# Kernel tuning notes

Measured on AMD Instinct MI355X. Metric: run time of the kernel, lower is better.

The kernel has to match this reference:

```python
import jax, jax.numpy as jnp
import numpy as np

ALPHA = 0.5
ITERATIONS = 10
N_CLASSES = 64


def setup_inputs() -> dict:
    key = jax.random.key(0)
    k1, k2, k3, k4 = jax.random.split(key, 4)
    d_in, d_emb = 512, 256
    n_support, n_query = 4096, 4096
    support = jax.random.normal(k1, (1, n_support, d_in), dtype=jnp.float32)
    query = jax.random.normal(k2, (1, n_query, d_in), dtype=jnp.float32)
    # encoder weight, scaled like a typical init so embeddings are O(1)
    W = jax.random.normal(k3, (d_in, d_emb), dtype=jnp.float32) / np.sqrt(d_in)
    support_labels = jax.random.randint(k4, (n_support,), 0, N_CLASSES, dtype=jnp.int64)
    return {"support": support, "query": query, "W": W, "support_labels": support_labels}


def reference(support, query, W, support_labels):
    n_support = support.shape[1]
    n_query = query.shape[1]
    d_in = support.shape[-1]

    # encoder: flatten episode dim, linear projection
    support_emb = support.reshape(-1, d_in) @ W        # [n_support, d_emb]
    query_emb = query.reshape(-1, d_in) @ W            # [n_query, d_emb]
    all_emb = jnp.concatenate([support_emb, query_emb], axis=0)  # [N, d_emb]

    # similarity graph and row-normalized adjacency
    similarity = all_emb @ all_emb.T                   # [N, N]
    adjacency = (similarity > 0.5).astype(jnp.float32)
    degree = adjacency.sum(axis=1, keepdims=True)
    degree = jnp.where(degree == 0, 1.0, degree)
    normalized = adjacency / degree                    # [N, N]

    # initial label matrix: one-hot for support rows, zeros for query rows
    support_onehot = jax.nn.one_hot(support_labels, N_CLASSES, dtype=jnp.float32)
    label_init = jnp.concatenate(
        [support_onehot, jnp.zeros((n_query, N_CLASSES), dtype=jnp.float32)], axis=0
    )  # [N, C]

    def step(_, labels):
        return (1.0 - ALPHA) * labels + ALPHA * (normalized @ labels)

    labels = jax.lax.fori_loop(0, ITERATIONS, step, label_init)
    query_labels = labels[n_support:]                  # [n_query, C]
    return query_labels
```

## Files before the change

kernel.cpp:

```cpp
#include <hip/hip_runtime.h>

#define NSUP 4096
#define NTOT 8192
#define DIN  512
#define DEMB 256
#define NCLS 64
#define PKS  8

typedef __attribute__((ext_vector_type(8))) short bf16x8;
typedef __attribute__((ext_vector_type(4))) float f32x4;
typedef __attribute__((ext_vector_type(4))) unsigned int u32x4;

__device__ inline unsigned short f2bf(float x) {
  unsigned int u = __builtin_bit_cast(unsigned int, x);
  u += 0x7FFFu + ((u >> 16) & 1u);
  return (unsigned short)(u >> 16);
}
__device__ inline float bf2f(unsigned short h) {
  unsigned int u = ((unsigned int)h) << 16;
  return __builtin_bit_cast(float, u);
}

__device__ inline size_t lfrag(int i, int c) {
  return (((size_t)(i >> 5) * (NCLS / 16) + (c >> 4)) * 64 +
          (c & 15) + 16 * ((i >> 3) & 3)) * 8 + (i & 7);
}

__global__ __launch_bounds__(256) void splitX(
    const float* __restrict__ support, const float* __restrict__ query,
    unsigned short* __restrict__ XhF, unsigned short* __restrict__ XlF) {
  int w = threadIdx.x >> 6, lane = threadIdx.x & 63;
  int row = blockIdx.x * 4 + w;
  const float* X = (row < NSUP) ? (support + (size_t)row * DIN)
                                : (query + (size_t)(row - NSUP) * DIN);
  const float4* p = (const float4*)(X + lane * 8);
  float4 a = p[0], b = p[1];
  float v[8] = {a.x, a.y, a.z, a.w, b.x, b.y, b.z, b.w};
  bf16x8 hv, lv;
  #pragma unroll
  for (int j = 0; j < 8; j++) {
    unsigned short h = f2bf(v[j]);
    hv[j] = (short)h;
    lv[j] = (short)f2bf(v[j] - bf2f(h));
  }
  size_t off = (((size_t)(row >> 4) * (DIN / 32) + (lane >> 2)) * 64 +
                (row & 15) + 16 * (lane & 3)) * 8;
  *reinterpret_cast<bf16x8*>(XhF + off) = hv;
  *reinterpret_cast<bf16x8*>(XlF + off) = lv;
}

__global__ __launch_bounds__(256) void splitW(
    const float* __restrict__ W, unsigned short* __restrict__ WhF,
    unsigned short* __restrict__ WlF) {
  int idx = blockIdx.x * 256 + threadIdx.x;
  int n = idx & 255, kb8 = idx >> 8;
  bf16x8 hv, lv;
  #pragma unroll
  for (int j = 0; j < 8; j++) {
    float v = W[(size_t)(kb8 * 8 + j) * DEMB + n];
    unsigned short h = f2bf(v);
    hv[j] = (short)h;
    lv[j] = (short)f2bf(v - bf2f(h));
  }
  size_t off = (((size_t)(n >> 4) * (DIN / 32) + (kb8 >> 2)) * 64 +
                (n & 15) + 16 * (kb8 & 3)) * 8;
  *reinterpret_cast<bf16x8*>(WhF + off) = hv;
  *reinterpret_cast<bf16x8*>(WlF + off) = lv;
}

__global__ __launch_bounds__(256) void emb_mfma(
    const unsigned short* __restrict__ XhF, const unsigned short* __restrict__ XlF,
    const unsigned short* __restrict__ WhF, const unsigned short* __restrict__ WlF,
    unsigned short* __restrict__ ehiF, unsigned short* __restrict__ eloF) {
  __shared__ float lds[4][16][65];
  int lane = threadIdx.x & 63, w = threadIdx.x >> 6;
  int l15 = lane & 15, lg = lane >> 4;
  int rowblk0 = blockIdx.x * 2;
  f32x4 acc[2][4] = {};
  for (int kb = 0; kb < DIN / 32; kb++) {
    bf16x8 ah[2], al[2], bh[4], bl[4];
    #pragma unroll
    for (int fm = 0; fm < 2; fm++) {
      size_t o = (((size_t)(rowblk0 + fm) * (DIN / 32) + kb) * 64 + lane) * 8;
      ah[fm] = *reinterpret_cast<const bf16x8*>(XhF + o);
      al[fm] = *reinterpret_cast<const bf16x8*>(XlF + o);
    }
    #pragma unroll
    for (int fn = 0; fn < 4; fn++) {
      size_t o = (((size_t)(w * 4 + fn) * (DIN / 32) + kb) * 64 + lane) * 8;
      bh[fn] = *reinterpret_cast<const bf16x8*>(WhF + o);
      bl[fn] = *reinterpret_cast<const bf16x8*>(WlF + o);
    }
    #pragma unroll
    for (int fm = 0; fm < 2; fm++)
      #pragma unroll
      for (int fn = 0; fn < 4; fn++) {
        acc[fm][fn] = __builtin_amdgcn_mfma_f32_16x16x32_bf16(ah[fm], bh[fn], acc[fm][fn], 0, 0, 0);
        acc[fm][fn] = __builtin_amdgcn_mfma_f32_16x16x32_bf16(ah[fm], bl[fn], acc[fm][fn], 0, 0, 0);
        acc[fm][fn] = __builtin_amdgcn_mfma_f32_16x16x32_bf16(al[fm], bh[fn], acc[fm][fn], 0, 0, 0);
        acc[fm][fn] = __builtin_amdgcn_mfma_f32_16x16x32_bf16(al[fm], bl[fn], acc[fm][fn], 0, 0, 0);
      }
  }
  for (int fm = 0; fm < 2; fm++) {
    #pragma unroll
    for (int fn = 0; fn < 4; fn++)
      #pragma unroll
      for (int r = 0; r < 4; r++)
        lds[w][lg * 4 + r][fn * 16 + l15] = acc[fm][fn][r];
    __syncthreads();
    #pragma unroll
    for (int cb = 0; cb < 2; cb++) {
      const float* src = &lds[w][l15][cb * 32 + lg * 8];
      bf16x8 hv, lv;
      #pragma unroll
      for (int j = 0; j < 8; j++) {
        float v = src[j];
        unsigned short h = f2bf(v);
        hv[j] = (short)h;
        lv[j] = (short)f2bf(v - bf2f(h));
      }
      size_t off = (((size_t)(rowblk0 + fm) * (DEMB / 32) + w * 2 + cb) * 64 + lane) * 8;
      *reinterpret_cast<bf16x8*>(ehiF + off) = hv;
      *reinterpret_cast<bf16x8*>(eloF + off) = lv;
    }
    __syncthreads();
  }
}

__global__ __launch_bounds__(256) void sim_kernel(
    const unsigned short* __restrict__ ehiF, const unsigned short* __restrict__ eloF,
    unsigned int* __restrict__ Apk) {
  int bid = (blockIdx.x & 7) * 260 + (blockIdx.x >> 3);
  int r = 2079 - bid;
  int j = (int)((sqrtf((float)(8 * r + 1)) - 1.0f) * 0.5f);
  while ((j + 1) * (j + 2) / 2 <= r) ++j;
  while (j * (j + 1) / 2 > r) --j;
  int by = 63 - j;
  int bx = 63 - (r - j * (j + 1) / 2);

  __shared__ unsigned short LTn[128][8];
  __shared__ unsigned short LTt[128][8];
  int lane = threadIdx.x & 63;
  int w = threadIdx.x >> 6, wm = w >> 1, wn = w & 1;
  int l15 = lane & 15, lg = lane >> 4;
  int arb = by * 8 + wm * 4, brb = bx * 8 + wn * 4;

  f32x4 acc[4][4] = {};
  #pragma unroll 2
  for (int kb = 0; kb < DEMB / 32; kb++) {
    bf16x8 bh[4], bl[4];
    #pragma unroll
    for (int fn = 0; fn < 4; fn++) {
      size_t o = (((size_t)(brb + fn) * (DEMB / 32) + kb) * 64 + lane) * 8;
      bh[fn] = *reinterpret_cast<const bf16x8*>(ehiF + o);
      bl[fn] = *reinterpret_cast<const bf16x8*>(eloF + o);
    }
    #pragma unroll
    for (int fm = 0; fm < 4; fm++) {
      size_t o = (((size_t)(arb + fm) * (DEMB / 32) + kb) * 64 + lane) * 8;
      bf16x8 ah = *reinterpret_cast<const bf16x8*>(ehiF + o);
      bf16x8 al = *reinterpret_cast<const bf16x8*>(eloF + o);
      #pragma unroll
      for (int fn = 0; fn < 4; fn++) {
        acc[fm][fn] = __builtin_amdgcn_mfma_f32_16x16x32_bf16(ah, bh[fn], acc[fm][fn], 0, 0, 0);
        acc[fm][fn] = __builtin_amdgcn_mfma_f32_16x16x32_bf16(ah, bl[fn], acc[fm][fn], 0, 0, 0);
        acc[fm][fn] = __builtin_amdgcn_mfma_f32_16x16x32_bf16(al, bh[fn], acc[fm][fn], 0, 0, 0);
      }
    }
  }
  #pragma unroll
  for (int fm = 0; fm < 4; fm++)
    #pragma unroll
    for (int fn = 0; fn < 4; fn++)
      #pragma unroll
      for (int r4 = 0; r4 < 4; r4++) {
        unsigned long long bal = __ballot(acc[fm][fn][r4] > 0.5f);
        if (l15 == 0)
          LTn[wm * 64 + fm * 16 + lg * 4 + r4][wn * 4 + fn] =
              (unsigned short)(bal >> (lg * 16));
      }
  __syncthreads();
  if (threadIdx.x < 64) {
    int tr = threadIdx.x >> 3, tc = threadIdx.x & 7;
    unsigned int m[16], t;
    #pragma unroll
    for (int q = 0; q < 16; q++) m[q] = LTn[tr * 16 + q][tc];
    #pragma unroll
    for (int i = 0; i < 8; i++) { t = ((m[i] >> 8) ^ m[i + 8]) & 0x00FFu; m[i + 8] ^= t; m[i] ^= t << 8; }
    #pragma unroll
    for (int g = 0; g < 16; g += 8)
      #pragma unroll
      for (int i = g; i < g + 4; i++) { t = ((m[i] >> 4) ^ m[i + 4]) & 0x0F0Fu; m[i + 4] ^= t; m[i] ^= t << 4; }
    #pragma unroll
    for (int g = 0; g < 16; g += 4)
      #pragma unroll
      for (int i = g; i < g + 2; i++) { t = ((m[i] >> 2) ^ m[i + 2]) & 0x3333u; m[i + 2] ^= t; m[i] ^= t << 2; }
    #pragma unroll
    for (int g = 0; g < 16; g += 2) { t = ((m[g] >> 1) ^ m[g + 1]) & 0x5555u; m[g + 1] ^= t; m[g] ^= t << 1; }
    #pragma unroll
    for (int q = 0; q < 16; q++) LTt[tc * 16 + q][tr] = (unsigned short)m[q];
  }
  __syncthreads();
  #pragma unroll
  for (int pass = 0; pass < 2; pass++) {
    int idx = pass * 256 + threadIdx.x;
    int rb4 = idx >> 6, ln = idx & 63;
    int lr = rb4 * 16 + (ln & 15), Lg = ln >> 4;
    unsigned int d = 0, d2 = 0;
    #pragma unroll
    for (int t = 0; t < 4; t++) {
      int bix = t * 4 + Lg;
      unsigned int u = LTn[lr][bix >> 1];
      d |= ((u >> ((bix & 1) * 8)) & 0xffu) << (t * 8);
      unsigned int u2 = LTt[lr][bix >> 1];
      d2 |= ((u2 >> ((bix & 1) * 8)) & 0xffu) << (t * 8);
    }
    Apk[((size_t)(by * 8 + rb4) * 64 + bx) * 64 + ln] = d;
    Apk[((size_t)(bx * 8 + rb4) * 64 + by) * 64 + ln] = d2;
  }
}

__global__ __launch_bounds__(256) void degree_kernel(
    const unsigned int* __restrict__ Apk, float* __restrict__ rdeg) {
  __shared__ int dg[4][16];
  int rowblk = blockIdx.x;
  int w = threadIdx.x >> 6, lane = threadIdx.x & 63;
  const unsigned int* base = Apk + (size_t)rowblk * 4096;
  int cnt = 0;
  #pragma unroll
  for (int s = 0; s < 16; s++) cnt += __popc(base[(w * 16 + s) * 64 + lane]);
  cnt += __shfl_xor(cnt, 16);
  cnt += __shfl_xor(cnt, 32);
  if (lane < 16) dg[w][lane] = cnt;
  __syncthreads();
  if (threadIdx.x < 16) {
    int c = dg[0][threadIdx.x] + dg[1][threadIdx.x] + dg[2][threadIdx.x] + dg[3][threadIdx.x];
    rdeg[rowblk * 16 + threadIdx.x] = (c == 0) ? 1.f : 1.f / (float)c;
  }
}

__global__ __launch_bounds__(256) void init_labels(
    const int* __restrict__ slab, float* __restrict__ labels,
    unsigned short* __restrict__ LtF) {
  int idx = blockIdx.x * 256 + threadIdx.x;
  int i = idx >> 6, c = idx & 63;
  float v = 0.f;
  if (i < NSUP && slab[i] == c) v = 1.f;
  labels[idx] = v;
  LtF[lfrag(i, c)] = f2bf(v);
}

#define RED(k, row, col) red[k][row][(col) ^ ((((row) >> 2) & 3) << 4)]
__global__ __launch_bounds__(512, 4) void prop_gemm(
    const unsigned int* __restrict__ Apk, const unsigned short* __restrict__ LtinF,
    float* __restrict__ Cpart) {
  __shared__ float red[4][64][64];
  int lane = threadIdx.x & 63;
  int w = threadIdx.x >> 6;
  int wr = w >> 2, wk = w & 3;
  int l15 = lane & 15, lg = lane >> 4;
  int ks = blockIdx.x, rg = blockIdx.y;
  int rb0 = rg * 8 + wr * 4;
  int s4base = ks * 8 + wk * 2;

  f32x4 acc[4][4] = {};
  #pragma unroll
  for (int s4 = 0; s4 < 2; s4++) {
    unsigned int ad[4];
    #pragma unroll
    for (int rb = 0; rb < 4; rb++)
      ad[rb] = Apk[((size_t)(rb0 + rb) * 64 + (s4base + s4)) * 64 + lane];
    #pragma unroll
    for (int t = 0; t < 4; t++) {
      int kstep = (s4base + s4) * 4 + t;
      bf16x8 b[4];
      #pragma unroll
      for (int fn = 0; fn < 4; fn++)
        b[fn] = *reinterpret_cast<const bf16x8*>(
            LtinF + (((size_t)kstep * 4 + fn) * 64 + lane) * 8);
      #pragma unroll
      for (int rb = 0; rb < 4; rb++) {
        unsigned int bb = (ad[rb] >> (8 * t)) & 0xffu;
        u32x4 uu;
        uu.x = ((bb & 1u)   ? 0x3F80u : 0u) | ((bb & 2u)   ? 0x3F800000u : 0u);
        uu.y = ((bb & 4u)   ? 0x3F80u : 0u) | ((bb & 8u)   ? 0x3F800000u : 0u);
        uu.z = ((bb & 16u)  ? 0x3F80u : 0u) | ((bb & 32u)  ? 0x3F800000u : 0u);
        uu.w = ((bb & 64u)  ? 0x3F80u : 0u) | ((bb & 128u) ? 0x3F800000u : 0u);
        bf16x8 a = __builtin_bit_cast(bf16x8, uu);
        #pragma unroll
        for (int fn = 0; fn < 4; fn++)
          acc[rb][fn] = __builtin_amdgcn_mfma_f32_16x16x32_bf16(a, b[fn], acc[rb][fn], 0, 0, 0);
      }
    }
  }
  float* cp = Cpart + (size_t)ks * (NTOT * NCLS);
  #pragma unroll
  for (int p = 0; p < 2; p++) {
    #pragma unroll
    for (int rbl = 0; rbl < 2; rbl++) {
      int rb = p * 2 + rbl;
      #pragma unroll
      for (int fn = 0; fn < 4; fn++)
        #pragma unroll
        for (int r4 = 0; r4 < 4; r4++)
          RED(wk, wr * 32 + rbl * 16 + lg * 4 + r4, fn * 16 + l15) = acc[rb][fn][r4];
    }
    __syncthreads();
    #pragma unroll
    for (int e = 0; e < 8; e++) {
      int idx = e * 512 + (int)threadIdx.x;
      int rr = idx >> 6, c = idx & 63;
      float s = RED(0, rr, c) + RED(1, rr, c) + RED(2, rr, c) + RED(3, rr, c);
      int grow = rg * 128 + (rr >> 5) * 64 + p * 32 + (rr & 31);
      cp[(size_t)grow * 64 + c] = s;
    }
    __syncthreads();
  }
}

__global__ __launch_bounds__(256) void prop_epi(
    const float* __restrict__ Cpart, const float* __restrict__ rdeg,
    float* __restrict__ labels, unsigned short* __restrict__ LtoutF,
    float* __restrict__ outq, int last) {
  __shared__ unsigned short stile[2048];
  int i_loc = threadIdx.x >> 3, c0 = (threadIdx.x & 7) * 8;
  int i = blockIdx.x * 32 + i_loc;
  int idx = i * NCLS + c0;
  float4 s0 = make_float4(0.f, 0.f, 0.f, 0.f), s1 = s0;
  #pragma unroll
  for (int k = 0; k < PKS; k++) {
    const float4* cp = (const float4*)(Cpart + (size_t)k * (NTOT * NCLS) + idx);
    float4 a = cp[0], b = cp[1];
    s0.x += a.x; s0.y += a.y; s0.z += a.z; s0.w += a.w;
    s1.x += b.x; s1.y += b.y; s1.z += b.z; s1.w += b.w;
  }
  float rd = 0.5f * rdeg[i];
  const float4* lp = (const float4*)(labels + idx);
  float4 l0 = lp[0], l1 = lp[1];
  float v[8];
  v[0] = 0.5f * l0.x + s0.x * rd;  v[1] = 0.5f * l0.y + s0.y * rd;
  v[2] = 0.5f * l0.z + s0.z * rd;  v[3] = 0.5f * l0.w + s0.w * rd;
  v[4] = 0.5f * l1.x + s1.x * rd;  v[5] = 0.5f * l1.y + s1.y * rd;
  v[6] = 0.5f * l1.z + s1.z * rd;  v[7] = 0.5f * l1.w + s1.w * rd;
  float4 o0 = make_float4(v[0], v[1], v[2], v[3]);
  float4 o1 = make_float4(v[4], v[5], v[6], v[7]);
  ((float4*)(labels + idx))[0] = o0;
  ((float4*)(labels + idx))[1] = o1;
  if (last && i >= NSUP) {
    float4* oq = (float4*)(outq + idx - NSUP * NCLS);
    oq[0] = o0; oq[1] = o1;
  }
  int sb = (c0 >> 4) * 512 + ((i_loc >> 3) & 3) * 128 + (i_loc & 7);
  #pragma unroll
  for (int jj = 0; jj < 8; jj++)
    stile[sb + ((c0 + jj) & 15) * 8] = f2bf(v[jj]);
  __syncthreads();
  *reinterpret_cast<bf16x8*>(LtoutF + (size_t)blockIdx.x * 2048 + threadIdx.x * 8) =
      *reinterpret_cast<const bf16x8*>(&stile[threadIdx.x * 8]);
}

extern "C" void kernel_launch(void* const* d_in, const int* in_sizes, int n_in,
                              void* d_out, int out_size, void* d_ws, size_t ws_size,
                              hipStream_t stream) {
  const float* support = (const float*)d_in[0];
  const float* query   = (const float*)d_in[1];
  const float* W       = (const float*)d_in[2];
  const int*   slab    = (const int*)d_in[3];
  float* out = (float*)d_out;
  char* ws = (char*)d_ws;
  const size_t MB = (size_t)1 << 20;
  unsigned short* XhF    = (unsigned short*)(ws);
  unsigned int*   Apk    = (unsigned int*)(ws);
  unsigned short* XlF    = (unsigned short*)(ws + 8 * MB);
  float*          Cpart  = (float*)(ws + 8 * MB);
  unsigned short* ehiF   = (unsigned short*)(ws + 24 * MB);
  unsigned short* eloF   = (unsigned short*)(ws + 28 * MB);
  unsigned short* WhF    = (unsigned short*)(ws + 32 * MB);
  unsigned short* WlF    = (unsigned short*)(ws + 32 * MB + 256 * 1024);
  float*          labels = (float*)(ws + 33 * MB);
  unsigned short* Lt0    = (unsigned short*)(ws + 35 * MB);
  unsigned short* Lt1    = (unsigned short*)(ws + 36 * MB);
  float*          rdeg   = (float*)(ws + 37 * MB);

  splitX<<<NTOT / 4, 256, 0, stream>>>(support, query, XhF, XlF);
  splitW<<<DIN * DEMB / 8 / 256, 256, 0, stream>>>(W, WhF, WlF);
  emb_mfma<<<NTOT / 32, 256, 0, stream>>>(XhF, XlF, WhF, WlF, ehiF, eloF);
  sim_kernel<<<2080, 256, 0, stream>>>(ehiF, eloF, Apk);
  degree_kernel<<<NTOT / 16, 256, 0, stream>>>(Apk, rdeg);
  init_labels<<<NTOT * NCLS / 256, 256, 0, stream>>>(slab, labels, Lt0);
  for (int t = 0; t < 10; t++) {
    unsigned short* Li = (t & 1) ? Lt1 : Lt0;
    unsigned short* Lo = (t & 1) ? Lt0 : Lt1;
    prop_gemm<<<dim3(PKS, 64), 512, 0, stream>>>(Apk, Li, Cpart);
    prop_epi<<<NTOT / 32, 256, 0, stream>>>(Cpart, rdeg, labels, Lo, out, (t == 9) ? 1 : 0);
  }
}
```

Before: 380.3 us.

## Fuse propagation GEMM and epilogue with in-block split-K reduction

Replaces the split-K propagation GEMM, which wrote 8 partial result slabs to global memory, plus its separate epilogue kernel with one fused kernel per iteration. Each block now owns 32 rows, and its 8 waves each cover one eighth of K. The partials are reduced in shared memory, then the label update and the bf16 fragment repack happen in place. This drops the 16MB partial-buffer write and read and one launch per iteration. In exchange, each block handles only 2 row-blocks, so the A-fragment reuse of each B load falls from 4 to 2 and B traffic to L2 roughly doubles. The grid also changes from 512 to 256 blocks.

```diff
diff --git a/kernel.cpp b/kernel.cpp
--- a/kernel.cpp
+++ b/kernel.cpp
@@ -5,7 +5,6 @@
 #define DIN  512
 #define DEMB 256
 #define NCLS 64
-#define PKS  8
 
 typedef __attribute__((ext_vector_type(8))) short bf16x8;
 typedef __attribute__((ext_vector_type(4))) float f32x4;
@@ -251,25 +250,25 @@
 }
 
 #define RED(k, row, col) red[k][row][(col) ^ ((((row) >> 2) & 3) << 4)]
-__global__ __launch_bounds__(512, 4) void prop_gemm(
+__global__ __launch_bounds__(512) void prop_fused(
     const unsigned int* __restrict__ Apk, const unsigned short* __restrict__ LtinF,
-    float* __restrict__ Cpart) {
-  __shared__ float red[4][64][64];
+    const float* __restrict__ rdeg, float* __restrict__ labels,
+    unsigned short* __restrict__ LtoutF, float* __restrict__ outq, int last) {
+  __shared__ float red[8][32][64];
+  __shared__ unsigned short stile[2048];
   int lane = threadIdx.x & 63;
-  int w = threadIdx.x >> 6;
-  int wr = w >> 2, wk = w & 3;
+  int wk = threadIdx.x >> 6;
   int l15 = lane & 15, lg = lane >> 4;
-  int ks = blockIdx.x, rg = blockIdx.y;
-  int rb0 = rg * 8 + wr * 4;
-  int s4base = ks * 8 + wk * 2;
-
-  f32x4 acc[4][4] = {};
-  #pragma unroll
-  for (int s4 = 0; s4 < 2; s4++) {
-    unsigned int ad[4];
-    #pragma unroll
-    for (int rb = 0; rb < 4; rb++)
-      ad[rb] = Apk[((size_t)(rb0 + rb) * 64 + (s4base + s4)) * 64 + lane];
+  int rg = blockIdx.x;
+  int rb0 = rg * 2;
+  int s4base = wk * 8;
+
+  f32x4 acc[2][4] = {};
+  #pragma unroll 2
+  for (int s4 = 0; s4 < 8; s4++) {
+    unsigned int ad[2];
+    ad[0] = Apk[((size_t)rb0 * 64 + s4base + s4) * 64 + lane];
+    ad[1] = Apk[((size_t)(rb0 + 1) * 64 + s4base + s4) * 64 + lane];
     #pragma unroll
     for (int t = 0; t < 4; t++) {
       int kstep = (s4base + s4) * 4 + t;
@@ -279,7 +278,7 @@
         b[fn] = *reinterpret_cast<const bf16x8*>(
             LtinF + (((size_t)kstep * 4 + fn) * 64 + lane) * 8);
       #pragma unroll
-      for (int rb = 0; rb < 4; rb++) {
+      for (int rb = 0; rb < 2; rb++) {
         unsigned int bb = (ad[rb] >> (8 * t)) & 0xffu;
         u32x4 uu;
         uu.x = ((bb & 1u)   ? 0x3F80u : 0u) | ((bb & 2u)   ? 0x3F800000u : 0u);
@@ -293,70 +292,43 @@
       }
     }
   }
-  float* cp = Cpart + (size_t)ks * (NTOT * NCLS);
-  #pragma unroll
-  for (int p = 0; p < 2; p++) {
-    #pragma unroll
-    for (int rbl = 0; rbl < 2; rbl++) {
-      int rb = p * 2 + rbl;
-      #pragma unroll
-      for (int fn = 0; fn < 4; fn++)
-        #pragma unroll
-        for (int r4 = 0; r4 < 4; r4++)
-          RED(wk, wr * 32 + rbl * 16 + lg * 4 + r4, fn * 16 + l15) = acc[rb][fn][r4];
-    }
-    __syncthreads();
-    #pragma unroll
-    for (int e = 0; e < 8; e++) {
-      int idx = e * 512 + (int)threadIdx.x;
-      int rr = idx >> 6, c = idx & 63;
-      float s = RED(0, rr, c) + RED(1, rr, c) + RED(2, rr, c) + RED(3, rr, c);
-      int grow = rg * 128 + (rr >> 5) * 64 + p * 32 + (rr & 31);
-      cp[(size_t)grow * 64 + c] = s;
-    }
-    __syncthreads();
-  }
-}
-
-__global__ __launch_bounds__(256) void prop_epi(
-    const float* __restrict__ Cpart, const float* __restrict__ rdeg,
-    float* __restrict__ labels, unsigned short* __restrict__ LtoutF,
-    float* __restrict__ outq, int last) {
-  __shared__ unsigned short stile[2048];
-  int i_loc = threadIdx.x >> 3, c0 = (threadIdx.x & 7) * 8;
-  int i = blockIdx.x * 32 + i_loc;
-  int idx = i * NCLS + c0;
-  float4 s0 = make_float4(0.f, 0.f, 0.f, 0.f), s1 = s0;
-  #pragma unroll
-  for (int k = 0; k < PKS; k++) {
-    const float4* cp = (const float4*)(Cpart + (size_t)k * (NTOT * NCLS) + idx);
-    float4 a = cp[0], b = cp[1];
-    s0.x += a.x; s0.y += a.y; s0.z += a.z; s0.w += a.w;
-    s1.x += b.x; s1.y += b.y; s1.z += b.z; s1.w += b.w;
-  }
-  float rd = 0.5f * rdeg[i];
-  const float4* lp = (const float4*)(labels + idx);
-  float4 l0 = lp[0], l1 = lp[1];
-  float v[8];
-  v[0] = 0.5f * l0.x + s0.x * rd;  v[1] = 0.5f * l0.y + s0.y * rd;
-  v[2] = 0.5f * l0.z + s0.z * rd;  v[3] = 0.5f * l0.w + s0.w * rd;
-  v[4] = 0.5f * l1.x + s1.x * rd;  v[5] = 0.5f * l1.y + s1.y * rd;
-  v[6] = 0.5f * l1.z + s1.z * rd;  v[7] = 0.5f * l1.w + s1.w * rd;
-  float4 o0 = make_float4(v[0], v[1], v[2], v[3]);
-  float4 o1 = make_float4(v[4], v[5], v[6], v[7]);
-  ((float4*)(labels + idx))[0] = o0;
-  ((float4*)(labels + idx))[1] = o1;
-  if (last && i >= NSUP) {
-    float4* oq = (float4*)(outq + idx - NSUP * NCLS);
-    oq[0] = o0; oq[1] = o1;
-  }
-  int sb = (c0 >> 4) * 512 + ((i_loc >> 3) & 3) * 128 + (i_loc & 7);
-  #pragma unroll
-  for (int jj = 0; jj < 8; jj++)
-    stile[sb + ((c0 + jj) & 15) * 8] = f2bf(v[jj]);
-  __syncthreads();
-  *reinterpret_cast<bf16x8*>(LtoutF + (size_t)blockIdx.x * 2048 + threadIdx.x * 8) =
-      *reinterpret_cast<const bf16x8*>(&stile[threadIdx.x * 8]);
+  #pragma unroll
+  for (int rb = 0; rb < 2; rb++)
+    #pragma unroll
+    for (int fn = 0; fn < 4; fn++)
+      #pragma unroll
+      for (int r4 = 0; r4 < 4; r4++)
+        RED(wk, rb * 16 + lg * 4 + r4, fn * 16 + l15) = acc[rb][fn][r4];
+  __syncthreads();
+  {
+    int row = threadIdx.x >> 4;
+    int c0 = (threadIdx.x & 15) * 4;
+    float s[4] = {0.f, 0.f, 0.f, 0.f};
+    #pragma unroll
+    for (int k = 0; k < 8; k++)
+      #pragma unroll
+      for (int jj = 0; jj < 4; jj++)
+        s[jj] += RED(k, row, c0 + jj);
+    int grow = rg * 32 + row;
+    size_t idx = (size_t)grow * NCLS + c0;
+    float rd = 0.5f * rdeg[grow];
+    float4 l = *reinterpret_cast<const float4*>(labels + idx);
+    float v0 = 0.5f * l.x + s[0] * rd, v1 = 0.5f * l.y + s[1] * rd;
+    float v2 = 0.5f * l.z + s[2] * rd, v3 = 0.5f * l.w + s[3] * rd;
+    float4 o = make_float4(v0, v1, v2, v3);
+    *reinterpret_cast<float4*>(labels + idx) = o;
+    if (last && grow >= NSUP)
+      *reinterpret_cast<float4*>(outq + idx - (size_t)NSUP * NCLS) = o;
+    int sb = (c0 >> 4) * 512 + ((row >> 3) & 3) * 128 + (row & 7);
+    stile[sb + ((c0 & 15) + 0) * 8] = f2bf(v0);
+    stile[sb + ((c0 & 15) + 1) * 8] = f2bf(v1);
+    stile[sb + ((c0 & 15) + 2) * 8] = f2bf(v2);
+    stile[sb + ((c0 & 15) + 3) * 8] = f2bf(v3);
+  }
+  __syncthreads();
+  if (threadIdx.x < 256)
+    *reinterpret_cast<bf16x8*>(LtoutF + (size_t)rg * 2048 + threadIdx.x * 8) =
+        *reinterpret_cast<const bf16x8*>(&stile[threadIdx.x * 8]);
 }
 
 extern "C" void kernel_launch(void* const* d_in, const int* in_sizes, int n_in,
@@ -372,7 +344,6 @@
   unsigned short* XhF    = (unsigned short*)(ws);
   unsigned int*   Apk    = (unsigned int*)(ws);
   unsigned short* XlF    = (unsigned short*)(ws + 8 * MB);
-  float*          Cpart  = (float*)(ws + 8 * MB);
   unsigned short* ehiF   = (unsigned short*)(ws + 24 * MB);
   unsigned short* eloF   = (unsigned short*)(ws + 28 * MB);
   unsigned short* WhF    = (unsigned short*)(ws + 32 * MB);
@@ -391,7 +362,6 @@
   for (int t = 0; t < 10; t++) {
     unsigned short* Li = (t & 1) ? Lt1 : Lt0;
     unsigned short* Lo = (t & 1) ? Lt0 : Lt1;
-    prop_gemm<<<dim3(PKS, 64), 512, 0, stream>>>(Apk, Li, Cpart);
-    prop_epi<<<NTOT / 32, 256, 0, stream>>>(Cpart, rdeg, labels, Lo, out, (t == 9) ? 1 : 0);
-  }
-}
+    prop_fused<<<NTOT / 32, 512, 0, stream>>>(Apk, Li, rdeg, labels, Lo, out, (t == 9) ? 1 : 0);
+  }
+}
```

Result: faster. 322.2 us (-15.3%).
